# Performance work log

Measured on AMD Instinct MI355X. Metric: run time of the kernel, lower is better.

Reference implementation:

```python
import jax, jax.numpy as jnp
import numpy as np

GROUPSIZE = 128
IN_F, OUT_F = 4096, 11008
TOKENS = 512


def setup_inputs() -> dict:
    key = jax.random.key(0)
    k1, k2, k3, k4, k5 = jax.random.split(key, 5)
    x = jax.random.normal(k1, (TOKENS, IN_F), dtype=jnp.float32)
    # packed 4-bit codes: two nibbles per byte, stored as int32 in [0, 256)
    qweight = jax.random.randint(k2, (OUT_F * IN_F // 2,), 0, 256, dtype=jnp.int32)
    n_groups = OUT_F * IN_F // GROUPSIZE
    scales = jax.random.uniform(k3, (n_groups, 1), dtype=jnp.float32) * 0.02 + 1e-3
    zeros = jax.random.uniform(k4, (n_groups, 1), dtype=jnp.float32) * 15.0
    bias = jax.random.normal(k5, (OUT_F,), dtype=jnp.float32)
    return {"x": x, "qweight": qweight, "scales": scales, "zeros": zeros, "bias": bias}


def _dequant_w4(qweight, scales, zeros, dtype):
    # python_decompress: high nibble then low nibble, each in [0,16)
    hi = (qweight >> 4) % 16
    lo = qweight % 16
    codes = jnp.stack([hi, lo], axis=-1).reshape(-1, GROUPSIZE).astype(dtype)
    # group-wise dequant: (code - zero) * scale, zeros/scales are (n_groups, 1)
    w = (codes - zeros.astype(dtype)) * scales.astype(dtype)
    return w.reshape(OUT_F, IN_F)


def reference(x, qweight, scales, zeros, bias):
    w = _dequant_w4(qweight, scales, zeros, x.dtype)  # [out, in]
    return x @ w.T + bias
```

## Files before the change

### kernel.cpp

```cpp
#include <hip/hip_runtime.h>

#define GROUPSIZE 128
#define IN_F 4096
#define OUT_F 11008
#define TOKENS 512
#define N_GROUPS (OUT_F * IN_F / GROUPSIZE)

#define BM 64
#define BN 128
#define BK 64
#define NTHREADS 256
#define NT (IN_F / BK)

typedef _Float16 half8  __attribute__((ext_vector_type(8)));
typedef _Float16 half2v __attribute__((ext_vector_type(2)));
typedef float    f32x4  __attribute__((ext_vector_type(4)));
typedef int      ivec4  __attribute__((ext_vector_type(4)));

__device__ __forceinline__ int swz(int r, int k) {
    return ((r << 6) + k) ^ ((r & 7) << 3);
}

__device__ __forceinline__ void glds16(const _Float16* g, _Float16* l) {
    __builtin_amdgcn_global_load_lds(
        (const __attribute__((address_space(1))) void*)g,
        (__attribute__((address_space(3))) void*)l, 16, 0, 0);
}

__global__ __launch_bounds__(256)
void cvt_x_kernel(const float* __restrict__ x, _Float16* __restrict__ x16) {
    size_t i = ((size_t)blockIdx.x * 256 + threadIdx.x) * 8;
    f32x4 a = *(const f32x4*)(x + i);
    f32x4 b = *(const f32x4*)(x + i + 4);
    half8 h;
    h[0]=(_Float16)a[0]; h[1]=(_Float16)a[1]; h[2]=(_Float16)a[2]; h[3]=(_Float16)a[3];
    h[4]=(_Float16)b[0]; h[5]=(_Float16)b[1]; h[6]=(_Float16)b[2]; h[7]=(_Float16)b[3];
    *(half8*)(x16 + i) = h;
}

__global__ __launch_bounds__(256)
void szpack_kernel(const float* __restrict__ s, const float* __restrict__ z,
                   uint2* __restrict__ szp) {
    int g = blockIdx.x * 256 + threadIdx.x;
    if (g >= N_GROUPS) return;
    _Float16 S = (_Float16)s[g];
    _Float16 B = (_Float16)(-(64.0f + z[g]) * (float)S);
    unsigned short su = __builtin_bit_cast(unsigned short, S);
    unsigned short bu = __builtin_bit_cast(unsigned short, B);
    uint2 r;
    r.x = ((unsigned)su << 16) | su;
    r.y = ((unsigned)bu << 16) | bu;
    szp[g] = r;
}

__device__ __forceinline__ half8 dq8(ivec4 q, uint2 sz) {
    half2v S  = __builtin_bit_cast(half2v, sz.x);
    half2v Bv = __builtin_bit_cast(half2v, sz.y);
    half8 r;
#pragma unroll
    for (int e = 0; e < 4; ++e) {
        unsigned qq = (unsigned)q[e];
        unsigned u = ((qq & 0xF0u) | ((qq << 20) & 0x00F00000u)) | 0x54005400u;
        half2v h = __builtin_bit_cast(half2v, u);
        half2v w = h * S + Bv;
        r[2*e]   = w[0];
        r[2*e+1] = w[1];
    }
    return r;
}

__global__ __launch_bounds__(NTHREADS, 3)
void qlinear_main(const _Float16* __restrict__ x16,
                  const int*   __restrict__ qw,
                  const uint2* __restrict__ szp,
                  const float* __restrict__ bias,
                  float*       __restrict__ out)
{
    __shared__ __align__(16) _Float16 As[2][BM * BK];
    __shared__ __align__(16) _Float16 Bs[2][BN * BK];

    const int tid = threadIdx.x;
    const int m0 = blockIdx.x * BM;
    const int n0 = blockIdx.y * BN;
    const int wv = tid >> 6, ln = tid & 63;

    const int s8 = tid & 7;
    const int r0 = tid >> 3;
    const int* qg = qw + (size_t)(n0 + r0) * (IN_F / 2) + s8 * 4;
    const int szb = (n0 + r0) * (IN_F / GROUPSIZE);

    const int ar  = wv * 16 + (ln >> 3);
    const int gsw = (ln & 7) ^ ((ln >> 3) & 7);
    const _Float16* ag = x16 + (size_t)(m0 + ar) * IN_F + gsw * 8;

    const int wr = (wv >> 1) * 32, wc = (wv & 1) * 64;
    const int lr = ln & 15, lk8 = (ln >> 4) * 8, lk4 = (ln >> 4) * 4;

    f32x4 acc[2][4];
#pragma unroll
    for (int i = 0; i < 2; ++i)
#pragma unroll
        for (int j = 0; j < 4; ++j)
            acc[i][j] = (f32x4){0.f, 0.f, 0.f, 0.f};

#define LOAD_Q(qs, szs, tt) do {                                            \
        _Pragma("unroll")                                                   \
        for (int j = 0; j < 4; ++j) {                                       \
            qs[j]  = *(const ivec4*)(qg + (size_t)j * 32 * (IN_F/2) + (tt) * 32); \
            szs[j] = szp[szb + j * 32 * (IN_F/GROUPSIZE) + ((tt) >> 1)];    \
        }                                                                   \
    } while (0)

#define STAGE_A(tt, buf) do {                                      \
        const _Float16* gp = ag + (size_t)(tt) * 64;               \
        glds16(gp,             &As[buf][wv * 1024]);               \
        glds16(gp + 8 * IN_F,  &As[buf][wv * 1024 + 512]);         \
    } while (0)

#define DQ_STORE(qs, szs, buf) do {                                        \
        _Pragma("unroll")                                                  \
        for (int j = 0; j < 4; ++j)                                        \
            *(half8*)&Bs[buf][swz(r0 + 32 * j, s8 * 8)] = dq8(qs[j], szs[j]); \
    } while (0)

    auto mfma_phase = [&](int buf) {
#pragma unroll
        for (int kk = 0; kk < 2; ++kk) {
            half8 af[2], bf[4];
#pragma unroll
            for (int i = 0; i < 2; ++i)
                af[i] = *(const half8*)&As[buf][swz(wr + i * 16 + lr, kk * 32 + lk8)];
#pragma unroll
            for (int j = 0; j < 4; ++j)
                bf[j] = *(const half8*)&Bs[buf][swz(wc + j * 16 + lr, kk * 32 + lk8)];
#pragma unroll
            for (int i = 0; i < 2; ++i)
#pragma unroll
                for (int j = 0; j < 4; ++j)
                    acc[i][j] = __builtin_amdgcn_mfma_f32_16x16x32_f16(
                        af[i], bf[j], acc[i][j], 0, 0, 0);
        }
    };

    ivec4 qA[4], qB[4];
    uint2 szA[4], szB[4];
    LOAD_Q(qA, szA, 0);
    LOAD_Q(qB, szB, 1);
    STAGE_A(0, 0);
    DQ_STORE(qA, szA, 0);
    __syncthreads();

    for (int t = 0; t < NT; t += 2) {
        {
            const int tl = (t + 2 < NT) ? t + 2 : NT - 1;
            LOAD_Q(qA, szA, tl);
            STAGE_A((t + 1 < NT) ? t + 1 : NT - 1, 1);
            DQ_STORE(qB, szB, 1);
            mfma_phase(0);
            __syncthreads();
        }
        {
            const int tl = (t + 3 < NT) ? t + 3 : NT - 1;
            LOAD_Q(qB, szB, tl);
            STAGE_A((t + 2 < NT) ? t + 2 : NT - 1, 0);
            DQ_STORE(qA, szA, 0);
            mfma_phase(1);
            __syncthreads();
        }
    }

#pragma unroll
    for (int j = 0; j < 4; ++j) {
        const int col = n0 + wc + j * 16 + lr;
        const float bv = bias[col];
#pragma unroll
        for (int i = 0; i < 2; ++i) {
            const int rb = m0 + wr + i * 16 + lk4;
#pragma unroll
            for (int r = 0; r < 4; ++r)
                out[(size_t)(rb + r) * OUT_F + col] = acc[i][j][r] + bv;
        }
    }
#undef LOAD_Q
#undef STAGE_A
#undef DQ_STORE
}

extern "C" void kernel_launch(void* const* d_in, const int* in_sizes, int n_in,
                              void* d_out, int out_size, void* d_ws, size_t ws_size,
                              hipStream_t stream) {
    const float* x      = (const float*)d_in[0];
    const int*   qw     = (const int*)d_in[1];
    const float* scales = (const float*)d_in[2];
    const float* zeros  = (const float*)d_in[3];
    const float* bias   = (const float*)d_in[4];
    float*       out    = (float*)d_out;

    _Float16* x16 = (_Float16*)d_ws;
    uint2*    szp = (uint2*)((char*)d_ws + (size_t)TOKENS * IN_F * 2);

    cvt_x_kernel<<<TOKENS * IN_F / (256 * 8), 256, 0, stream>>>(x, x16);
    szpack_kernel<<<(N_GROUPS + 255) / 256, 256, 0, stream>>>(scales, zeros, szp);

    dim3 grid(TOKENS / BM, OUT_F / BN);
    qlinear_main<<<grid, NTHREADS, 0, stream>>>(x16, qw, szp, bias, out);
}
```

Baseline: 255.0 us.

## Split-K with atomics, packed nibbles in LDS, dequant at MFMA time, XCD-aware tiling

The main kernel is restructured in several ways. It splits K into two halves whose partial sums are combined with atomicAdd into an output pre-initialised with bias by a new kernel. It stores packed 4-bit codes in LDS rather than dequantized halves and dequantizes them with byte-permute ops inside the MFMA loop. Scales and zeros are transposed so they load coalesced, and tiles are remapped by XCD so each die reuses weight tiles. The intent is lower LDS traffic, higher occupancy and better L2 locality. The cost is float atomics, an extra kernel launch and more ALU work in the inner loop.

```diff
diff --git a/kernel.cpp b/kernel.cpp
--- a/kernel.cpp
+++ b/kernel.cpp
@@ -5,12 +5,15 @@
 #define OUT_F 11008
 #define TOKENS 512
 #define N_GROUPS (OUT_F * IN_F / GROUPSIZE)
+#define NGK (IN_F / GROUPSIZE)
 
 #define BM 64
 #define BN 128
 #define BK 64
 #define NTHREADS 256
-#define NT (IN_F / BK)
+#define NT_G (IN_F / BK)
+#define NT_H (NT_G / 2)
+#define NTILES_N (OUT_F / BN)
 
 typedef _Float16 half8  __attribute__((ext_vector_type(8)));
 typedef _Float16 half2v __attribute__((ext_vector_type(2)));
@@ -25,6 +28,32 @@
     __builtin_amdgcn_global_load_lds(
         (const __attribute__((address_space(1))) void*)g,
         (__attribute__((address_space(3))) void*)l, 16, 0, 0);
+}
+
+__device__ __forceinline__ unsigned pack4(ivec4 q) {
+    unsigned p01 = __builtin_amdgcn_perm((unsigned)q[1], (unsigned)q[0], 0x0C0C0400u);
+    unsigned p23 = __builtin_amdgcn_perm((unsigned)q[3], (unsigned)q[2], 0x0C0C0400u);
+    return __builtin_amdgcn_perm(p23, p01, 0x05040100u);
+}
+
+__device__ __forceinline__ half8 dqp(unsigned p, uint2 sz) {
+    unsigned A4 = (p << 4) & 0xF0F0F0F0u;
+    unsigned Bn =  p       & 0xF0F0F0F0u;
+    unsigned t01 = __builtin_amdgcn_perm(A4, Bn, 0x05010400u);
+    unsigned t23 = __builtin_amdgcn_perm(A4, Bn, 0x07030602u);
+    const unsigned k54 = 0x54545454u;
+    unsigned u0 = __builtin_amdgcn_perm(t01, k54, 0x00050004u);
+    unsigned u1 = __builtin_amdgcn_perm(t01, k54, 0x00070006u);
+    unsigned u2 = __builtin_amdgcn_perm(t23, k54, 0x00050004u);
+    unsigned u3 = __builtin_amdgcn_perm(t23, k54, 0x00070006u);
+    half2v S  = __builtin_bit_cast(half2v, sz.x);
+    half2v Bv = __builtin_bit_cast(half2v, sz.y);
+    union { half8 h; half2v p2[4]; } r;
+    r.p2[0] = __builtin_bit_cast(half2v, u0) * S + Bv;
+    r.p2[1] = __builtin_bit_cast(half2v, u1) * S + Bv;
+    r.p2[2] = __builtin_bit_cast(half2v, u2) * S + Bv;
+    r.p2[3] = __builtin_bit_cast(half2v, u3) * S + Bv;
+    return r.h;
 }
 
 __global__ __launch_bounds__(256)
@@ -40,9 +69,10 @@
 
 __global__ __launch_bounds__(256)
 void szpack_kernel(const float* __restrict__ s, const float* __restrict__ z,
-                   uint2* __restrict__ szp) {
+                   uint2* __restrict__ szt) {
     int g = blockIdx.x * 256 + threadIdx.x;
     if (g >= N_GROUPS) return;
+    int row = g / NGK, gk = g % NGK;
     _Float16 S = (_Float16)s[g];
     _Float16 B = (_Float16)(-(64.0f + z[g]) * (float)S);
     unsigned short su = __builtin_bit_cast(unsigned short, S);
@@ -50,140 +80,150 @@
     uint2 r;
     r.x = ((unsigned)su << 16) | su;
     r.y = ((unsigned)bu << 16) | bu;
-    szp[g] = r;
-}
-
-__device__ __forceinline__ half8 dq8(ivec4 q, uint2 sz) {
-    half2v S  = __builtin_bit_cast(half2v, sz.x);
-    half2v Bv = __builtin_bit_cast(half2v, sz.y);
-    half8 r;
-#pragma unroll
-    for (int e = 0; e < 4; ++e) {
-        unsigned qq = (unsigned)q[e];
-        unsigned u = ((qq & 0xF0u) | ((qq << 20) & 0x00F00000u)) | 0x54005400u;
-        half2v h = __builtin_bit_cast(half2v, u);
-        half2v w = h * S + Bv;
-        r[2*e]   = w[0];
-        r[2*e+1] = w[1];
-    }
-    return r;
-}
-
-__global__ __launch_bounds__(NTHREADS, 3)
+    szt[(size_t)gk * OUT_F + row] = r;
+}
+
+__global__ __launch_bounds__(256)
+void out_init_kernel(const float* __restrict__ bias, float* __restrict__ out) {
+    size_t i = ((size_t)blockIdx.x * 256 + threadIdx.x) * 4;
+    int col = (int)(i % OUT_F);
+    *(f32x4*)(out + i) = *(const f32x4*)(bias + col);
+}
+
+__global__ __launch_bounds__(NTHREADS, 4)
 void qlinear_main(const _Float16* __restrict__ x16,
                   const int*   __restrict__ qw,
-                  const uint2* __restrict__ szp,
-                  const float* __restrict__ bias,
+                  const uint2* __restrict__ szt,
                   float*       __restrict__ out)
 {
     __shared__ __align__(16) _Float16 As[2][BM * BK];
-    __shared__ __align__(16) _Float16 Bs[2][BN * BK];
+    __shared__ __align__(16) unsigned Qs[2][BN * BK / 8];
+
+    const int bid = blockIdx.x;
+    const int xcd = bid & 7;
+    const int sgrp = bid >> 3;
+    const int n_t = 11 * xcd + (sgrp >> 4);
+    const int sub = sgrp & 15;
+    const int m_t = sub & 7;
+    const int kh  = sub >> 3;
+    if (n_t >= NTILES_N) return;
+    const int n0 = n_t * BN, m0 = m_t * BM;
+    const int t0 = kh * NT_H;
 
     const int tid = threadIdx.x;
-    const int m0 = blockIdx.x * BM;
-    const int n0 = blockIdx.y * BN;
     const int wv = tid >> 6, ln = tid & 63;
 
-    const int s8 = tid & 7;
-    const int r0 = tid >> 3;
-    const int* qg = qw + (size_t)(n0 + r0) * (IN_F / 2) + s8 * 4;
-    const int szb = (n0 + r0) * (IN_F / GROUPSIZE);
+    const int s8 = tid & 7, r0 = tid >> 3;
+    const int* qg = qw + (size_t)(n0 + r0) * (IN_F / 2) + (size_t)t0 * 32 + s8 * 4;
+    const int dwp = s8 ^ ((r0 >> 2) & 3);
 
     const int ar  = wv * 16 + (ln >> 3);
     const int gsw = (ln & 7) ^ ((ln >> 3) & 7);
-    const _Float16* ag = x16 + (size_t)(m0 + ar) * IN_F + gsw * 8;
-
-    const int wr = (wv >> 1) * 32, wc = (wv & 1) * 64;
-    const int lr = ln & 15, lk8 = (ln >> 4) * 8, lk4 = (ln >> 4) * 4;
-
-    f32x4 acc[2][4];
-#pragma unroll
-    for (int i = 0; i < 2; ++i)
-#pragma unroll
-        for (int j = 0; j < 4; ++j)
+    const _Float16* ag = x16 + (size_t)(m0 + ar) * IN_F + (size_t)t0 * BK + gsw * 8;
+
+    const int wc2 = wv * 32;
+    const int lr = ln & 15, ln4 = ln >> 4, lk8 = ln4 * 8, lk4 = ln4 * 4;
+    int qrd[2][2];
+#pragma unroll
+    for (int j = 0; j < 2; ++j) {
+        int row = wc2 + j * 16 + lr;
+        int qx = (row >> 2) & 3;
+#pragma unroll
+        for (int kk = 0; kk < 2; ++kk)
+            qrd[j][kk] = row * 8 + ((kk * 4 + ln4) ^ qx);
+    }
+    const int szrow = n0 + wc2 + lr;
+
+    f32x4 acc[4][2];
+#pragma unroll
+    for (int i = 0; i < 4; ++i)
+#pragma unroll
+        for (int j = 0; j < 2; ++j)
             acc[i][j] = (f32x4){0.f, 0.f, 0.f, 0.f};
 
-#define LOAD_Q(qs, szs, tt) do {                                            \
+#define LOAD_Q(qs, tt) do {                                                 \
         _Pragma("unroll")                                                   \
-        for (int j = 0; j < 4; ++j) {                                       \
-            qs[j]  = *(const ivec4*)(qg + (size_t)j * 32 * (IN_F/2) + (tt) * 32); \
-            szs[j] = szp[szb + j * 32 * (IN_F/GROUPSIZE) + ((tt) >> 1)];    \
-        }                                                                   \
+        for (int j = 0; j < 4; ++j)                                         \
+            qs[j] = *(const ivec4*)(qg + (size_t)j * 32 * (IN_F/2) + (tt) * 32); \
     } while (0)
 
-#define STAGE_A(tt, buf) do {                                      \
-        const _Float16* gp = ag + (size_t)(tt) * 64;               \
-        glds16(gp,             &As[buf][wv * 1024]);               \
-        glds16(gp + 8 * IN_F,  &As[buf][wv * 1024 + 512]);         \
+#define STAGE_A(tt, buf) do {                                               \
+        const _Float16* gp = ag + (size_t)(tt) * 64;                        \
+        glds16(gp,            &As[buf][wv * 1024]);                         \
+        glds16(gp + 8 * IN_F, &As[buf][wv * 1024 + 512]);                   \
     } while (0)
 
-#define DQ_STORE(qs, szs, buf) do {                                        \
-        _Pragma("unroll")                                                  \
-        for (int j = 0; j < 4; ++j)                                        \
-            *(half8*)&Bs[buf][swz(r0 + 32 * j, s8 * 8)] = dq8(qs[j], szs[j]); \
+#define PACK_STORE(qs, buf) do {                                            \
+        _Pragma("unroll")                                                   \
+        for (int j = 0; j < 4; ++j)                                         \
+            Qs[buf][(r0 + 32 * j) * 8 + dwp] = pack4(qs[j]);                \
     } while (0)
 
-    auto mfma_phase = [&](int buf) {
+    uint2 szc0, szc1;
+
+    auto mfma_phase = [&](int b) {
 #pragma unroll
         for (int kk = 0; kk < 2; ++kk) {
-            half8 af[2], bf[4];
-#pragma unroll
-            for (int i = 0; i < 2; ++i)
-                af[i] = *(const half8*)&As[buf][swz(wr + i * 16 + lr, kk * 32 + lk8)];
-#pragma unroll
-            for (int j = 0; j < 4; ++j)
-                bf[j] = *(const half8*)&Bs[buf][swz(wc + j * 16 + lr, kk * 32 + lk8)];
-#pragma unroll
-            for (int i = 0; i < 2; ++i)
-#pragma unroll
-                for (int j = 0; j < 4; ++j)
-                    acc[i][j] = __builtin_amdgcn_mfma_f32_16x16x32_f16(
-                        af[i], bf[j], acc[i][j], 0, 0, 0);
+            half8 af[4];
+#pragma unroll
+            for (int i = 0; i < 4; ++i)
+                af[i] = *(const half8*)&As[b][swz(i * 16 + lr, kk * 32 + lk8)];
+            {
+                half8 bf = dqp(Qs[b][qrd[0][kk]], szc0);
+#pragma unroll
+                for (int i = 0; i < 4; ++i)
+                    acc[i][0] = __builtin_amdgcn_mfma_f32_16x16x32_f16(af[i], bf, acc[i][0], 0, 0, 0);
+            }
+            {
+                half8 bf = dqp(Qs[b][qrd[1][kk]], szc1);
+#pragma unroll
+                for (int i = 0; i < 4; ++i)
+                    acc[i][1] = __builtin_amdgcn_mfma_f32_16x16x32_f16(af[i], bf, acc[i][1], 0, 0, 0);
+            }
         }
     };
 
-    ivec4 qA[4], qB[4];
-    uint2 szA[4], szB[4];
-    LOAD_Q(qA, szA, 0);
-    LOAD_Q(qB, szB, 1);
-    STAGE_A(0, 0);
-    DQ_STORE(qA, szA, 0);
-    __syncthreads();
-
-    for (int t = 0; t < NT; t += 2) {
-        {
-            const int tl = (t + 2 < NT) ? t + 2 : NT - 1;
-            LOAD_Q(qA, szA, tl);
-            STAGE_A((t + 1 < NT) ? t + 1 : NT - 1, 1);
-            DQ_STORE(qB, szB, 1);
-            mfma_phase(0);
-            __syncthreads();
-        }
-        {
-            const int tl = (t + 3 < NT) ? t + 3 : NT - 1;
-            LOAD_Q(qB, szB, tl);
-            STAGE_A((t + 2 < NT) ? t + 2 : NT - 1, 0);
-            DQ_STORE(qA, szA, 0);
-            mfma_phase(1);
-            __syncthreads();
-        }
-    }
-
-#pragma unroll
-    for (int j = 0; j < 4; ++j) {
-        const int col = n0 + wc + j * 16 + lr;
-        const float bv = bias[col];
-#pragma unroll
-        for (int i = 0; i < 2; ++i) {
-            const int rb = m0 + wr + i * 16 + lk4;
+    ivec4 qr[4];
+    {
+        int gk0 = t0 >> 1;
+        szc0 = szt[(size_t)gk0 * OUT_F + szrow];
+        szc1 = szt[(size_t)gk0 * OUT_F + szrow + 16];
+        STAGE_A(0, 0);
+        LOAD_Q(qr, 0);
+        PACK_STORE(qr, 0);
+        asm volatile("s_waitcnt vmcnt(0) lgkmcnt(0)" ::: "memory");
+        __builtin_amdgcn_s_barrier();
+    }
+
+    for (int t = 0; t < NT_H; ++t) {
+        const int b = t & 1;
+        const int tn = (t + 1 < NT_H) ? t + 1 : NT_H - 1;
+        const int gkn = (t0 + tn) >> 1;
+        uint2 szn0 = szt[(size_t)gkn * OUT_F + szrow];
+        uint2 szn1 = szt[(size_t)gkn * OUT_F + szrow + 16];
+        STAGE_A(tn, b ^ 1);
+        LOAD_Q(qr, tn);
+        mfma_phase(b);
+        PACK_STORE(qr, b ^ 1);
+        asm volatile("s_waitcnt lgkmcnt(0)" ::: "memory");
+        __builtin_amdgcn_s_barrier();
+        szc0 = szn0; szc1 = szn1;
+    }
+
+#pragma unroll
+    for (int j = 0; j < 2; ++j) {
+        const int col = n0 + wc2 + j * 16 + lr;
+#pragma unroll
+        for (int i = 0; i < 4; ++i) {
+            const int rb = m0 + i * 16 + lk4;
 #pragma unroll
             for (int r = 0; r < 4; ++r)
-                out[(size_t)(rb + r) * OUT_F + col] = acc[i][j][r] + bv;
+                atomicAdd(&out[(size_t)(rb + r) * OUT_F + col], acc[i][j][r]);
         }
     }
 #undef LOAD_Q
 #undef STAGE_A
-#undef DQ_STORE
+#undef PACK_STORE
 }
 
 extern "C" void kernel_launch(void* const* d_in, const int* in_sizes, int n_in,
@@ -197,11 +237,11 @@
     float*       out    = (float*)d_out;
 
     _Float16* x16 = (_Float16*)d_ws;
-    uint2*    szp = (uint2*)((char*)d_ws + (size_t)TOKENS * IN_F * 2);
+    uint2*    szt = (uint2*)((char*)d_ws + (size_t)TOKENS * IN_F * 2);
 
     cvt_x_kernel<<<TOKENS * IN_F / (256 * 8), 256, 0, stream>>>(x, x16);
-    szpack_kernel<<<(N_GROUPS + 255) / 256, 256, 0, stream>>>(scales, zeros, szp);
-
-    dim3 grid(TOKENS / BM, OUT_F / BN);
-    qlinear_main<<<grid, NTHREADS, 0, stream>>>(x16, qw, szp, bias, out);
-}
+    szpack_kernel<<<(N_GROUPS + 255) / 256, 256, 0, stream>>>(scales, zeros, szt);
+    out_init_kernel<<<TOKENS * OUT_F / (256 * 4), 256, 0, stream>>>(bias, out);
+
+    qlinear_main<<<1408, NTHREADS, 0, stream>>>(x16, qw, szt, out);
+}
```

New measurement: 256.9 us. No clear change (+0.7%).
